# Kernel tuning notes

Hardware: AMD Instinct MI355X
Metric: run time of the kernel (lower is better)

Reference implementation:

```python
import jax, jax.numpy as jnp
import numpy as np

B, T, NB = 8192, 18, 6
EH, DH = 256, 256
NIN = NB + 1  # encoder GRU input: bits + feedback scalar


def gru_cell(x, h, Wih, Whh, bih, bhh):
    # PyTorch GRU cell: gates ordered (r, z, n)
    gi = x @ Wih.T + bih
    gh = h @ Whh.T + bhh
    ir, iz, inn = jnp.split(gi, 3, axis=-1)
    hr, hz, hn = jnp.split(gh, 3, axis=-1)
    r = jax.nn.sigmoid(ir + hr)
    z = jax.nn.sigmoid(iz + hz)
    n = jnp.tanh(inn + r * hn)
    return (1.0 - z) * n + z * h


def run_gru_dir(seq, Wih, Whh, bih, bhh, reverse):
    # seq: [T, B, D] -> hidden outputs [T, B, H] (aligned to original time order)
    Bn, H = seq.shape[1], Whh.shape[1]
    def step(h, x):
        h2 = gru_cell(x, h, Wih, Whh, bih, bhh)
        return h2, h2
    _, outs = jax.lax.scan(step, jnp.zeros((Bn, H), seq.dtype), seq, reverse=reverse)
    return outs


def setup_inputs() -> dict:
    key = jax.random.key(0)
    ks = jax.random.split(key, 40)
    def w(k, shape, fan):
        s = 1.0 / np.sqrt(fan)
        return jax.random.uniform(k, shape, jnp.float32, -s, s)
    inp = {}
    inp['b'] = (jax.random.uniform(ks[0], (B, NB)) < 0.5).astype(jnp.float32)
    inp['noise1'] = jax.random.normal(ks[1], (B, T, 1), jnp.float32)
    inp['noise2'] = jax.random.normal(ks[2], (B, T, 1), jnp.float32)
    # encoder GRU (2 layers, unidirectional)
    inp['enc_Wih0'] = w(ks[3], (3 * EH, NIN), EH); inp['enc_Whh0'] = w(ks[4], (3 * EH, EH), EH)
    inp['enc_bih0'] = w(ks[5], (3 * EH,), EH);     inp['enc_bhh0'] = w(ks[6], (3 * EH,), EH)
    inp['enc_Wih1'] = w(ks[7], (3 * EH, EH), EH);  inp['enc_Whh1'] = w(ks[8], (3 * EH, EH), EH)
    inp['enc_bih1'] = w(ks[9], (3 * EH,), EH);     inp['enc_bhh1'] = w(ks[10], (3 * EH,), EH)
    inp['enc_lin_W'] = w(ks[11], (1, EH), EH);     inp['enc_lin_b'] = w(ks[12], (1,), EH)
    inp['weight_power'] = jnp.ones((T,), jnp.float32)
    # decoder GRU (2 layers, bidirectional)
    inp['dec_Wih0f'] = w(ks[13], (3 * DH, 1), DH);      inp['dec_Whh0f'] = w(ks[14], (3 * DH, DH), DH)
    inp['dec_bih0f'] = w(ks[15], (3 * DH,), DH);        inp['dec_bhh0f'] = w(ks[16], (3 * DH,), DH)
    inp['dec_Wih0b'] = w(ks[17], (3 * DH, 1), DH);      inp['dec_Whh0b'] = w(ks[18], (3 * DH, DH), DH)
    inp['dec_bih0b'] = w(ks[19], (3 * DH,), DH);        inp['dec_bhh0b'] = w(ks[20], (3 * DH,), DH)
    inp['dec_Wih1f'] = w(ks[21], (3 * DH, 2 * DH), DH); inp['dec_Whh1f'] = w(ks[22], (3 * DH, DH), DH)
    inp['dec_bih1f'] = w(ks[23], (3 * DH,), DH);        inp['dec_bhh1f'] = w(ks[24], (3 * DH,), DH)
    inp['dec_Wih1b'] = w(ks[25], (3 * DH, 2 * DH), DH); inp['dec_Whh1b'] = w(ks[26], (3 * DH, DH), DH)
    inp['dec_bih1b'] = w(ks[27], (3 * DH,), DH);        inp['dec_bhh1b'] = w(ks[28], (3 * DH,), DH)
    inp['dec_lin_W'] = w(ks[29], (NB, 2 * DH), 2 * DH); inp['dec_lin_b'] = w(ks[30], (NB,), 2 * DH)
    inp['weight_merge'] = jnp.ones((T, 2), jnp.float32)
    return inp


def reference(b, noise1, noise2,
              enc_Wih0, enc_Whh0, enc_bih0, enc_bhh0,
              enc_Wih1, enc_Whh1, enc_bih1, enc_bhh1,
              enc_lin_W, enc_lin_b, weight_power,
              dec_Wih0f, dec_Whh0f, dec_bih0f, dec_bhh0f,
              dec_Wih0b, dec_Whh0b, dec_bih0b, dec_bhh0b,
              dec_Wih1f, dec_Whh1f, dec_bih1f, dec_bhh1f,
              dec_Wih1b, dec_Whh1b, dec_bih1b, dec_bhh1b,
              dec_lin_W, dec_lin_b, weight_merge):
    Bn = b.shape[0]
    Tn = weight_power.shape[0]
    # power-normalized per-step weights: sqrt(w^2 * T / sum(w^2))
    wp = jnp.sqrt(weight_power ** 2 * Tn / jnp.sum(weight_power ** 2))

    def enc_step(carry, xs):
        h0, h1, z = carry
        n1, n2, wpt = xs
        inp = jnp.concatenate([b, z], axis=1)            # [B, NB+1]
        h0n = gru_cell(inp, h0, enc_Wih0, enc_Whh0, enc_bih0, enc_bhh0)
        h1n = gru_cell(h0n, h1, enc_Wih1, enc_Whh1, enc_bih1, enc_bhh1)
        xt = jnp.tanh(h1n @ enc_lin_W.T + enc_lin_b)     # [B, 1]
        xn = (xt - jnp.mean(xt)) / jnp.std(xt, ddof=1)   # training-mode batch norm over whole tensor
        y = xn * wpt + n1                                # received symbol
        return (h0n, h1n, y + n2), y                     # feedback z = y + noise2

    carry0 = (jnp.zeros((Bn, EH), b.dtype), jnp.zeros((Bn, EH), b.dtype), jnp.zeros((Bn, 1), b.dtype))
    xs = (jnp.swapaxes(noise1, 0, 1), jnp.swapaxes(noise2, 0, 1), wp)
    _, y_seq = jax.lax.scan(enc_step, carry0, xs)        # [T, B, 1]

    # bidirectional 2-layer decoder GRU over y
    o0f = run_gru_dir(y_seq, dec_Wih0f, dec_Whh0f, dec_bih0f, dec_bhh0f, False)
    o0b = run_gru_dir(y_seq, dec_Wih0b, dec_Whh0b, dec_bih0b, dec_bhh0b, True)
    s1 = jnp.concatenate([o0f, o0b], axis=-1)            # [T, B, 2*DH]
    o1f = run_gru_dir(s1, dec_Wih1f, dec_Whh1f, dec_bih1f, dec_bhh1f, False)
    o1b = run_gru_dir(s1, dec_Wih1b, dec_Whh1b, dec_bih1b, dec_bhh1b, True)

    # attention_type == 5: learned weighted merge over time, per direction
    wf = jnp.sqrt(weight_merge[:, 0] ** 2 * Tn / jnp.sum(weight_merge[:, 0] ** 2))
    wb = jnp.sqrt(weight_merge[:, 1] ** 2 * Tn / jnp.sum(weight_merge[:, 1] ** 2))
    rf = jnp.einsum('tbh,t->bh', o1f, wf)
    rb = jnp.einsum('tbh,t->bh', o1b, wb)
    rc = jnp.concatenate([rf, rb], axis=1)               # [B, 2*DH]
    out = jax.nn.sigmoid(rc @ dec_lin_W.T + dec_lin_b)   # bit_vector output -> sigmoid
    return out.reshape(Bn, -1, 1)
```

## Files before the change

### kernel.cpp

```cpp
#include <hip/hip_runtime.h>
#include <hip/hip_bf16.h>
#include <math.h>

#define BN_ 8192
#define TT 18
#define NBITS 6
#define HH 256
#define G3 768

typedef __hip_bfloat16 hbf16;
typedef __bf16 bf16x8 __attribute__((ext_vector_type(8)));
typedef float f32x4 __attribute__((ext_vector_type(4)));

__device__ inline float sigm(float x){ return 1.0f/(1.0f + __expf(-x)); }
__device__ inline float ftanh(float x){ float e = __expf(2.0f*x); return 1.0f - 2.0f/(e + 1.0f); }
__device__ inline float ldx(const void* p, int i, int bf){
    if(bf){ unsigned short u = ((const unsigned short*)p)[i]; return __uint_as_float(((unsigned)u)<<16); }
    return ((const float*)p)[i];
}
__device__ inline __bf16 f2b(float f){ hbf16 h = __float2bfloat16(f); return *reinterpret_cast<__bf16*>(&h); }
__device__ inline float b2f(__bf16 b){ unsigned short u = *reinterpret_cast<unsigned short*>(&b); return __uint_as_float(((unsigned)u)<<16); }
__device__ inline unsigned pack2(float a, float b){
    hbf16 lo = __float2bfloat16(a), hi = __float2bfloat16(b);
    return (unsigned)*(unsigned short*)&lo | ((unsigned)*(unsigned short*)&hi << 16);
}

__device__ __forceinline__ void gld_lds16(const void* g, void* l){
    __builtin_amdgcn_global_load_lds(
        (const __attribute__((address_space(1))) unsigned int*)g,
        (__attribute__((address_space(3))) unsigned int*)l, 16, 0, 0);
}

__global__ __launch_bounds__(256) void fillz(float* __restrict__ p, int n){
    for(int i = blockIdx.x*256 + threadIdx.x; i < n; i += gridDim.x*256) p[i] = 0.0f;
}
__global__ __launch_bounds__(256) void fillb(__bf16* __restrict__ p, int n){
    for(int i = blockIdx.x*256 + threadIdx.x; i < n; i += gridDim.x*256) p[i] = f2b(0.0f);
}

__global__ void prep_w(const void* wp, const void* wm, unsigned* flag,
                       float* wpn, float* wfn, float* wbn){
    if(threadIdx.x==0 && blockIdx.x==0){
        unsigned w0 = *(const unsigned*)wp;
        int bf = ((w0 >> 16) == (w0 & 0xFFFFu)) ? 1 : 0;
        flag[0] = (unsigned)bf;
        float s=0; for(int t=0;t<TT;t++){ float v=ldx(wp,t,bf); s += v*v; }
        for(int t=0;t<TT;t++){ float v=ldx(wp,t,bf); wpn[t] = sqrtf(v*v*TT/s); }
        float sf=0, sb=0;
        for(int t=0;t<TT;t++){ float f=ldx(wm,2*t,bf), b=ldx(wm,2*t+1,bf); sf += f*f; sb += b*b; }
        for(int t=0;t<TT;t++){
            float f=ldx(wm,2*t,bf), b=ldx(wm,2*t+1,bf);
            wfn[t] = sqrtf(f*f*TT/sf);
            wbn[t] = sqrtf(b*b*TT/sb);
        }
    }
}

struct CJ { const void* src; void* dst; int n; int K; int mode; };
struct CJs { CJ j[20]; };
__global__ __launch_bounds__(256) void conv_all(CJs J, const unsigned* __restrict__ flagp){
    const int bf = (int)*flagp;
    CJ c = J.j[blockIdx.y];
    for(int i = blockIdx.x*256 + threadIdx.x; i < c.n; i += gridDim.x*256){
        if(c.mode==1){
            int row = i / c.K, k = i - row*c.K;
            int g = row>>8, jj = row&255;
            int prow = ((jj>>4)*48) + g*16 + (jj&15);
            ((__bf16*)c.dst)[(size_t)prow*c.K + k] = f2b(ldx(c.src, i, bf));
        }else if(c.mode==2){
            int t = i >> 13, b = i & (BN_-1);
            ((float*)c.dst)[i] = ldx(c.src, b*TT + t, bf);
        }else{
            ((float*)c.dst)[i] = ldx(c.src, i, bf);
        }
    }
}

struct FQ {
    const __bf16* A1; const __bf16* W1; int K1;
    const __bf16* A2; const __bf16* W2; int K2;
    const float* bgi; const float* bgh;
    const __bf16* h; __bf16* hout;
    const void* bits; const void* wih0raw; const void* bih0raw;
    const void* linw; float* xt;
    const float* y; const void* wihraw; const void* bihraw; __bf16* s1t;
    float* racc; const float* wct;
};
struct FQ2 { FQ q[2]; };

template<int MODE>
__global__ __launch_bounds__(256,4) void fused_step(FQ2 PP, const unsigned* __restrict__ flagp){
    const FQ P = PP.q[blockIdx.z];
    const int bf = (int)*flagp;
    constexpr int BM   = (MODE<=1) ? 64 : 128;
    constexpr int NF   = BM/32;
    constexpr int ABYT = BM*64;
    constexpr int BUFB = ABYT + 6144;
    __shared__ __align__(16) char smem[28672];
    __shared__ float zs[192];
    __shared__ float sred[4], ssred[4];
    float*  T  = (float*)smem;
    const int tid = threadIdx.x;
    constexpr int MTS = (8192/BM)/8;
    const int mt = blockIdx.x*MTS + (blockIdx.y>>3);
    const int jt = blockIdx.y & 7;
    const int m0 = mt*BM;
    const int n0 = jt*96;
    const int lane = tid&63, wv = tid>>6;
    const int wvbase = tid & ~63;
    const int wrow = wv>>1, wcol = wv&1;
    const int q = lane>>4, n15 = lane&15;

    constexpr int S1  = (MODE==1) ? 8 : (MODE==3 ? 16 : 0);
    constexpr int NST = S1 + 8;
    constexpr int KD1 = (MODE==3) ? 512 : 256;
    constexpr int KD2 = 256;
    const __bf16* pA1 = (S1>0) ? P.A1 + (size_t)m0*KD1 : (const __bf16*)nullptr;
    const __bf16* pW1 = (S1>0) ? P.W1 + (size_t)n0*KD1 : (const __bf16*)nullptr;
    const __bf16* pA2 = P.A2 + (size_t)m0*KD2;
    const __bf16* pW2 = P.W2 + (size_t)n0*KD2;
    const int r0 = tid>>2, sl0 = tid&3;
    const int q0 = sl0 ^ ((r0>>1)&3);
    const int r1 = 64 + r0;
    const int q1 = sl0 ^ ((r1>>1)&3);

    auto STG = [&](int s){
        const __bf16* A; const __bf16* W; int K; int k0;
        if(s < S1){ A = pA1; W = pW1; K = KD1; k0 = s*32; }
        else      { A = pA2; W = pW2; K = KD2; k0 = (s-S1)*32; }
        char* buf = smem + (s&1)*BUFB;
        gld_lds16(A + (size_t)r0*K + k0 + q0*8, buf + (size_t)wvbase*16);
        if constexpr(BM==128)
            gld_lds16(A + (size_t)r1*K + k0 + q1*8, buf + (size_t)(256+wvbase)*16);
        gld_lds16(W + (size_t)r0*K + k0 + q0*8, buf + ABYT + (size_t)wvbase*16);
        if(tid < 128)
            gld_lds16(W + (size_t)r1*K + k0 + q1*8, buf + ABYT + (size_t)(256+wvbase)*16);
    };

    STG(0);

    if(MODE==0){
        if(P.K1){
            const float lbv = ldx(P.linw, 0, bf);
            const float wt  = P.wct[0];
            const float* __restrict__ xr = P.xt;
            float s=0.0f, ss=0.0f;
            const float4* x4 = (const float4*)xr;
            for(int i=tid;i<BN_/4;i+=256){
                float4 vv = x4[i];
                float a0=ftanh(vv.x+lbv), a1=ftanh(vv.y+lbv), a2=ftanh(vv.z+lbv), a3=ftanh(vv.w+lbv);
                s += a0+a1+a2+a3; ss += a0*a0+a1*a1+a2*a2+a3*a3;
            }
            #pragma unroll
            for(int o=32;o;o>>=1){ s += __shfl_xor(s,o); ss += __shfl_xor(ss,o); }
            if(lane==0){ sred[wv]=s; ssred[wv]=ss; }
            __syncthreads();
            float a = sred[0]+sred[1]+sred[2]+sred[3];
            float bq = ssred[0]+ssred[1]+ssred[2]+ssred[3];
            float mean = a/(float)BN_;
            float var = (bq - (float)BN_*mean*mean)/(float)(BN_-1);
            float rs = 1.0f/sqrtf(var);
            if(tid<BM){
                int row = m0 + tid;
                float v = ftanh(xr[row]+lbv);
                float yv = (v-mean)*rs*wt + P.y[row];
                zs[tid] = yv + ((const float*)P.wihraw)[row];
                if(jt==0){ ((float*)P.s1t)[row] = yv; P.racc[row] = 0.0f; }
            }
        }else{
            if(tid<BM) zs[tid] = 0.0f;
        }
        __syncthreads();
    }else{
        __syncthreads();
    }

    f32x4 accR[NF], accZ[NF], accN1[NF], accN2[NF];
    #pragma unroll
    for(int i=0;i<NF;i++){ accR[i]=(f32x4){0,0,0,0}; accZ[i]=(f32x4){0,0,0,0};
                           accN1[i]=(f32x4){0,0,0,0}; accN2[i]=(f32x4){0,0,0,0}; }

    #pragma unroll
    for(int s=0; s<NST; ++s){
        if(s+1 < NST) STG(s+1);
        const char* buf = smem + (s&1)*BUFB;
        const __bf16* Asb = (const __bf16*)buf;
        const __bf16* Wsb = (const __bf16*)(buf + ABYT);
        bf16x8 af[NF], bfr[3];
        #pragma unroll
        for(int i=0;i<NF;i++){
            int R = wrow*(BM/2)+i*16+n15;
            int col = q ^ ((R>>1)&3);
            af[i] = *(const bf16x8*)&Asb[R*32 + col*8];
        }
        #pragma unroll
        for(int g=0;g<3;g++){
            int RW = wcol*48+g*16+n15;
            int col = q ^ ((RW>>1)&3);
            bfr[g] = *(const bf16x8*)&Wsb[RW*32 + col*8];
        }
        #pragma unroll
        for(int i=0;i<NF;i++){
            accR[i] = __builtin_amdgcn_mfma_f32_16x16x32_bf16(af[i], bfr[0], accR[i], 0,0,0);
            accZ[i] = __builtin_amdgcn_mfma_f32_16x16x32_bf16(af[i], bfr[1], accZ[i], 0,0,0);
            if(s < S1) accN1[i] = __builtin_amdgcn_mfma_f32_16x16x32_bf16(af[i], bfr[2], accN1[i], 0,0,0);
            else       accN2[i] = __builtin_amdgcn_mfma_f32_16x16x32_bf16(af[i], bfr[2], accN2[i], 0,0,0);
        }
        __syncthreads();
    }

    const int jl = wcol*16 + n15;
    const int j  = jt*32 + jl;
    const float bghr = P.bgh[j], bghz = P.bgh[256+j], bghn = P.bgh[512+j];
    float bgir=0, bgiz=0, bgin=0;
    if(MODE==1 || MODE==3){ bgir = P.bgi[j]; bgiz = P.bgi[256+j]; bgin = P.bgi[512+j]; }
    float w0r[7], w0z[7], w0n[7];
    if(MODE==0){
        #pragma unroll
        for(int k=0;k<7;k++){
            w0r[k] = ldx(P.wih0raw, (j    )*7+k, bf);
            w0z[k] = ldx(P.wih0raw, (j+256)*7+k, bf);
            w0n[k] = ldx(P.wih0raw, (j+512)*7+k, bf);
        }
        bgir = ldx(P.bih0raw, j, bf); bgiz = ldx(P.bih0raw, j+256, bf); bgin = ldx(P.bih0raw, j+512, bf);
    }
    float wy_r=0, wy_z=0, wy_n=0;
    if(MODE==2){
        wy_r = ldx(P.wihraw, j, bf); wy_z = ldx(P.wihraw, j+256, bf); wy_n = ldx(P.wihraw, j+512, bf);
        bgir = ldx(P.bihraw, j, bf); bgiz = ldx(P.bihraw, j+256, bf); bgin = ldx(P.bihraw, j+512, bf);
    }
    const float linwj = (MODE==1) ? ldx(P.linw, j, bf) : 0.0f;

    #pragma unroll
    for(int i=0;i<NF;i++){
        const int rbl = wrow*(BM/2) + i*16 + q*4;
        float vred[4];
        #pragma unroll
        for(int r=0;r<4;r++){
            const int row_l = rbl + r;
            const int row = m0 + row_l;
            float gir, giz, gin;
            if(MODE==1 || MODE==3){
                gir = bgir; giz = bgiz; gin = accN1[i][r] + bgin;
            }else if(MODE==0){
                gir = bgir; giz = bgiz; gin = bgin;
                #pragma unroll
                for(int k=0;k<NBITS;k++){
                    float bv = ldx(P.bits, row*NBITS+k, bf);
                    gir += bv*w0r[k]; giz += bv*w0z[k]; gin += bv*w0n[k];
                }
                float zb = zs[row_l];
                gir += zb*w0r[6]; giz += zb*w0z[6]; gin += zb*w0n[6];
            }else{
                float yv = P.y[row];
                gir = yv*wy_r + bgir; giz = yv*wy_z + bgiz; gin = yv*wy_n + bgin;
            }
            float rr = sigm(gir + accR[i][r] + bghr);
            float zz = sigm(giz + accZ[i][r] + bghz);
            float nn = ftanh(gin + rr*(accN2[i][r] + bghn));
            float hold = b2f(P.h[(size_t)row*HH + j]);
            float hn = (1.0f - zz)*nn + zz*hold;
            T[row_l*33 + jl] = hn;
            if(MODE==1) vred[r] = hn*linwj;
        }
        if(MODE==1){
            #pragma unroll
            for(int r=0;r<4;r++){
                float v = vred[r];
                #pragma unroll
                for(int m=1;m<16;m<<=1) v += __shfl_xor(v, m);
                if(n15==0) atomicAdd(&P.xt[m0+rbl+r], v);
            }
        }
    }
    if(MODE==3 && tid<192){
        int k = tid>>5, jj = tid&31;
        zs[tid] = ldx(P.bits, k*512 + (int)blockIdx.z*256 + jt*32 + jj, bf);
    }
    __syncthreads();

    const int rw2 = tid>>2, cw = tid&3;
    #pragma unroll
    for(int pass=0; pass<BM/64; pass++){
        const int row_l = pass*64 + rw2;
        const int row = m0 + row_l;
        float v[8];
        #pragma unroll
        for(int u=0;u<8;u++) v[u] = T[row_l*33 + cw*8 + u];
        uint4 pkv = { pack2(v[0],v[1]), pack2(v[2],v[3]), pack2(v[4],v[5]), pack2(v[6],v[7]) };
        *(uint4*)&P.hout[(size_t)row*HH + jt*32 + cw*8] = pkv;
        if(MODE==2) *(uint4*)&P.s1t[(size_t)row*512 + jt*32 + cw*8] = pkv;
    }
    if(MODE==3){
        float* pp = P.xt + (size_t)(jt + 8*(int)blockIdx.z)*(BN_*NBITS);
        const float wct3 = P.wct[0];
        #pragma unroll
        for(int u=0;u<3;u++){
            int idx = tid + 256*u;
            int row_l = idx/6, k = idx - row_l*6;
            float dot = 0.0f;
            #pragma unroll
            for(int jj=0;jj<32;jj++) dot += T[row_l*33+jj]*zs[k*32+jj];
            size_t gi = (size_t)(m0+row_l)*NBITS + k;
            pp[gi] += wct3*dot;
        }
    }
}

__global__ __launch_bounds__(1024) void stats_emit(float* __restrict__ xt, const void* __restrict__ lb,
        const float* __restrict__ wpn, int t, const float* __restrict__ n1t, const float* __restrict__ n2t,
        float* __restrict__ yseq, float* __restrict__ zf, const unsigned* __restrict__ flagp){
    const int bf = (int)*flagp;
    const float lbv = ldx(lb, 0, bf);
    int tid = threadIdx.x;
    float s=0.0f, ss=0.0f;
    for(int i=tid;i<BN_;i+=1024){ float v = ftanh(xt[i] + lbv); s += v; ss += v*v; }
    #pragma unroll
    for(int o=32;o;o>>=1){ s += __shfl_down(s,o); ss += __shfl_down(ss,o); }
    __shared__ float S[16], SS[16], stm[2];
    if((tid&63)==0){ S[tid>>6]=s; SS[tid>>6]=ss; }
    __syncthreads();
    if(tid==0){
        float a=0.0f, b=0.0f;
        for(int i=0;i<16;i++){ a+=S[i]; b+=SS[i]; }
        float mean = a/(float)BN_;
        float var = (b - (float)BN_*mean*mean)/(float)(BN_-1);
        stm[0]=mean; stm[1]=1.0f/sqrtf(var);
    }
    __syncthreads();
    const float mean=stm[0], rs=stm[1], wt=wpn[t];
    for(int i=tid;i<BN_;i+=1024){
        float v = ftanh(xt[i] + lbv);
        float y = (v-mean)*rs*wt + n1t[i];
        yseq[(size_t)t*BN_ + i] = y;
        zf[i] = y + n2t[i];
        xt[i] = 0.0f;
    }
}

__global__ __launch_bounds__(256) void out_head(const float* __restrict__ pp, const void* __restrict__ bias,
        void* __restrict__ out, const unsigned* __restrict__ flagp){
    const int bf = (int)*flagp;
    int i = blockIdx.x*256 + threadIdx.x;
    if(i >= BN_*NBITS) return;
    float s = 0.0f;
    #pragma unroll
    for(int k=0;k<16;k++) s += pp[(size_t)k*(BN_*NBITS) + i];
    int kk = i - (i/6)*6;
    float v = sigm(s + ldx(bias, kk, bf));
    if(bf) ((hbf16*)out)[i] = __float2bfloat16(v);
    else   ((float*)out)[i] = v;
}

extern "C" void kernel_launch(void* const* d_in, const int* in_sizes, int n_in,
                              void* d_out, int out_size, void* d_ws, size_t ws_size,
                              hipStream_t stream)
{
    (void)in_sizes; (void)n_in; (void)out_size;
    const void* bits  = d_in[0];
    const void* n1    = d_in[1];
    const void* n2    = d_in[2];
    const void* eWih0 = d_in[3];
    const void* eWhh0 = d_in[4];
    const void* ebih0 = d_in[5];
    const void* ebhh0 = d_in[6];
    const void* eWih1 = d_in[7];
    const void* eWhh1 = d_in[8];
    const void* ebih1 = d_in[9];
    const void* ebhh1 = d_in[10];
    const void* elinW = d_in[11];
    const void* elinb = d_in[12];
    const void* wpow  = d_in[13];
    const void* dWih0f= d_in[14];
    const void* dWhh0f= d_in[15];
    const void* dbih0f= d_in[16];
    const void* dbhh0f= d_in[17];
    const void* dWih0b= d_in[18];
    const void* dWhh0b= d_in[19];
    const void* dbih0b= d_in[20];
    const void* dbhh0b= d_in[21];
    const void* dWih1f= d_in[22];
    const void* dWhh1f= d_in[23];
    const void* dbih1f= d_in[24];
    const void* dbhh1f= d_in[25];
    const void* dWih1b= d_in[26];
    const void* dWhh1b= d_in[27];
    const void* dbih1b= d_in[28];
    const void* dbhh1b= d_in[29];
    const void* dlinW = d_in[30];
    const void* dlinb = d_in[31];
    const void* wmrg  = d_in[32];

    float* base = (float*)d_ws;
    size_t off = 0;
    auto alloc  = [&](size_t n){ float* p = base + off; off += (n + 63) & ~(size_t)63; return p; };
    auto allocb = [&](size_t n){ __bf16* p = (__bf16*)(base + off); off += ((n/2) + 63) & ~(size_t)63; return p; };
    unsigned* flag = (unsigned*)alloc(64);
    float* wpn = alloc(TT); float* wfn = alloc(TT); float* wbn = alloc(TT);
    const int WK = HH*G3;
    __bf16* WeHH0 = allocb(WK);  __bf16* WeIH1 = allocb(WK);  __bf16* WeHH1 = allocb(WK);
    __bf16* Wd0f  = allocb(WK);  __bf16* Wd0b  = allocb(WK);
    __bf16* Wd1fI = allocb(2*WK);__bf16* Wd1bI = allocb(2*WK);
    __bf16* Wd1fH = allocb(WK);  __bf16* Wd1bH = allocb(WK);
    float* BeHH0 = alloc(G3); float* BeIH1 = alloc(G3); float* BeHH1 = alloc(G3);
    float* Bd0f  = alloc(G3); float* Bd0b  = alloc(G3);
    float* Bd1fI = alloc(G3); float* Bd1bI = alloc(G3);
    float* Bd1fH = alloc(G3); float* Bd1bH = alloc(G3);
    const size_t NH = (size_t)BN_*HH;
    __bf16* X0 = allocb(NH);  __bf16* X1 = allocb(NH);
    __bf16* Y0 = allocb(NH);  __bf16* Y1 = allocb(NH);
    float* pout = alloc((size_t)16*BN_*NBITS);
    float* xtA = alloc(BN_);
    float* xtB = alloc(BN_);
    float* zf  = alloc(BN_);
    float* yseq= alloc((size_t)TT*BN_);
    float* n1t = alloc((size_t)TT*BN_);
    float* n2t = alloc((size_t)TT*BN_);
    __bf16* s1 = allocb((size_t)TT*BN_*512);
    size_t need = off*sizeof(float);
    if(ws_size < need) return;

    prep_w<<<1,64,0,stream>>>(wpow, wmrg, flag, wpn, wfn, wbn);
    CJs J;
    const void* ws_src[20] = {eWhh0,eWih1,eWhh1,dWhh0f,dWhh0b,dWih1f,dWih1b,dWhh1f,dWhh1b,
                              ebhh0,ebih1,ebhh1,dbhh0f,dbhh0b,dbih1f,dbih1b,dbhh1f,dbhh1b, n1, n2};
    void* ws_dst[20] = {WeHH0,WeIH1,WeHH1,Wd0f,Wd0b,Wd1fI,Wd1bI,Wd1fH,Wd1bH,
                        BeHH0,BeIH1,BeHH1,Bd0f,Bd0b,Bd1fI,Bd1bI,Bd1fH,Bd1bH, n1t, n2t};
    int ws_n[20] = {WK,WK,WK,WK,WK,2*WK,2*WK,WK,WK, G3,G3,G3,G3,G3,G3,G3,G3,G3, TT*BN_, TT*BN_};
    int ws_K[20] = {256,256,256,256,256,512,512,256,256, 0,0,0,0,0,0,0,0,0, 0,0};
    int ws_m[20] = {1,1,1,1,1,1,1,1,1, 0,0,0,0,0,0,0,0,0, 2,2};
    for(int i=0;i<20;i++){ J.j[i] = {ws_src[i], ws_dst[i], ws_n[i], ws_K[i], ws_m[i]}; }
    conv_all<<<dim3(768,20),256,0,stream>>>(J, flag);
    fillb<<<1024,256,0,stream>>>(X0, (int)NH);
    fillb<<<1024,256,0,stream>>>(Y0, (int)NH);
    fillz<<<32,256,0,stream>>>(xtA, BN_);
    fillz<<<32,256,0,stream>>>(xtB, BN_);
    fillz<<<192,256,0,stream>>>(pout, 16*BN_*NBITS);

    dim3 g1(8, 128, 1), g2(8, 64, 2);
    __bf16* X[2] = {X0, X1};
    __bf16* Y[2] = {Y0, Y1};
    float* xts[2] = {xtA, xtB};

    int p = 0;
    for(int t=0;t<TT;t++){
        FQ2 P0{}; FQ2 P1{};
        FQ& a = P0.q[0];
        a.A2=X[p]; a.W2=WeHH0; a.K2=HH; a.bgh=BeHH0; a.h=X[p]; a.hout=X[1-p];
        a.bits=bits; a.wih0raw=eWih0; a.bih0raw=ebih0;
        a.K1 = (t>0) ? 1 : 0;
        if(t>0){
            a.xt   = xts[(t-1)&1];
            a.racc = xts[t&1];
            a.y    = n1t + (size_t)(t-1)*BN_;
            a.wihraw = (const void*)(n2t + (size_t)(t-1)*BN_);
            a.s1t  = (__bf16*)(yseq + (size_t)(t-1)*BN_);
            a.wct  = wpn + (t-1);
            a.linw = elinb;
        }
        fused_step<0><<<g1,256,0,stream>>>(P0, flag);
        FQ& b = P1.q[0];
        b.A1=X[1-p]; b.W1=WeIH1; b.K1=HH; b.A2=Y[p]; b.W2=WeHH1; b.K2=HH;
        b.bgi=BeIH1; b.bgh=BeHH1; b.h=Y[p]; b.hout=Y[1-p];
        b.linw=elinW; b.xt=xts[t&1];
        fused_step<1><<<g1,256,0,stream>>>(P1, flag);
        p ^= 1;
    }
    stats_emit<<<1,1024,0,stream>>>(xts[(TT-1)&1], elinb, wpn, TT-1,
                                    n1t+(size_t)(TT-1)*BN_, n2t+(size_t)(TT-1)*BN_, yseq, zf, flag);

    fillb<<<1024,256,0,stream>>>(X0, (int)NH);
    fillb<<<1024,256,0,stream>>>(Y0, (int)NH);
    p = 0;
    for(int i=0;i<TT;i++){
        int tf = i, tb = TT-1-i;
        FQ2 P{};
        FQ& a = P.q[0];
        a.A2=X[p]; a.W2=Wd0f; a.K2=HH; a.bgh=Bd0f; a.h=X[p]; a.hout=X[1-p];
        a.y=yseq+(size_t)tf*BN_; a.wihraw=dWih0f; a.bihraw=dbih0f; a.s1t=s1+(size_t)tf*BN_*512;
        FQ& b = P.q[1];
        b.A2=Y[p]; b.W2=Wd0b; b.K2=HH; b.bgh=Bd0b; b.h=Y[p]; b.hout=Y[1-p];
        b.y=yseq+(size_t)tb*BN_; b.wihraw=dWih0b; b.bihraw=dbih0b; b.s1t=s1+(size_t)tb*BN_*512+256;
        fused_step<2><<<g2,256,0,stream>>>(P, flag);
        p ^= 1;
    }

    fillb<<<1024,256,0,stream>>>(X0, (int)NH);
    fillb<<<1024,256,0,stream>>>(Y0, (int)NH);
    p = 0;
    for(int i=0;i<TT;i++){
        int tf = i, tb = TT-1-i;
        FQ2 P{};
        FQ& a = P.q[0];
        a.A1=s1+(size_t)tf*BN_*512; a.W1=Wd1fI; a.K1=512;
        a.A2=X[p]; a.W2=Wd1fH; a.K2=HH; a.bgi=Bd1fI; a.bgh=Bd1fH; a.h=X[p]; a.hout=X[1-p];
        a.bits=dlinW; a.xt=pout; a.wct=wfn+tf;
        FQ& b = P.q[1];
        b.A1=s1+(size_t)tb*BN_*512; b.W1=Wd1bI; b.K1=512;
        b.A2=Y[p]; b.W2=Wd1bH; b.K2=HH; b.bgi=Bd1bI; b.bgh=Bd1bH; b.h=Y[p]; b.hout=Y[1-p];
        b.bits=dlinW; b.xt=pout; b.wct=wbn+tb;
        fused_step<3><<<g2,256,0,stream>>>(P, flag);
        p ^= 1;
    }

    out_head<<<192,256,0,stream>>>(pout, dlinb, d_out, flag);
}
```

Baseline: 1.698 ms.

## Widen decoder GRU step tiles to 512 threads covering 64 hidden units

For the decoder modes, each block now runs 512 threads (8 waves) and covers 192 gate columns (64 hidden units) instead of 96, halving the number of column tiles per row tile. A-operand tiles of batch rows are reloaded half as often, and the partial-output buffer for the bit-projection shrinks from 16 to 8 slices. The cost is more shared memory and registers per block, which may reduce occupancy under the launch bounds.

```diff
diff --git a/kernel.cpp b/kernel.cpp
--- a/kernel.cpp
+++ b/kernel.cpp
@@ -89,26 +89,33 @@
 struct FQ2 { FQ q[2]; };
 
 template<int MODE>
-__global__ __launch_bounds__(256,4) void fused_step(FQ2 PP, const unsigned* __restrict__ flagp){
+__global__ __launch_bounds__((MODE>=2)?512:256, 4) void fused_step(FQ2 PP, const unsigned* __restrict__ flagp){
     const FQ P = PP.q[blockIdx.z];
     const int bf = (int)*flagp;
+    constexpr int THREADS = (MODE>=2) ? 512 : 256;
     constexpr int BM   = (MODE<=1) ? 64 : 128;
+    constexpr int WR   = (MODE>=2) ? 192 : 96;
+    constexpr int JB   = WR/3;
     constexpr int NF   = BM/32;
     constexpr int ABYT = BM*64;
-    constexpr int BUFB = ABYT + 6144;
-    __shared__ __align__(16) char smem[28672];
-    __shared__ float zs[192];
+    constexpr int WBYT = WR*64;
+    constexpr int BUFB = ABYT + WBYT;
+    constexpr int TS   = JB + 1;
+    __shared__ __align__(16) char smem[2*BUFB];
+    __shared__ float zs[(MODE>=2)?384:192];
     __shared__ float sred[4], ssred[4];
     float*  T  = (float*)smem;
     const int tid = threadIdx.x;
+    constexpr int JTBITS = (MODE>=2) ? 2 : 3;
     constexpr int MTS = (8192/BM)/8;
-    const int mt = blockIdx.x*MTS + (blockIdx.y>>3);
-    const int jt = blockIdx.y & 7;
+    const int mt = blockIdx.x*MTS + (blockIdx.y>>JTBITS);
+    const int jt = blockIdx.y & ((1<<JTBITS)-1);
     const int m0 = mt*BM;
-    const int n0 = jt*96;
+    const int n0 = jt*WR;
     const int lane = tid&63, wv = tid>>6;
     const int wvbase = tid & ~63;
-    const int wrow = wv>>1, wcol = wv&1;
+    const int wrow = (MODE>=2) ? (wv>>2) : (wv>>1);
+    const int wcol = wv & ((MODE>=2)?3:1);
     const int q = lane>>4, n15 = lane&15;
 
     constexpr int S1  = (MODE==1) ? 8 : (MODE==3 ? 16 : 0);
@@ -121,8 +128,8 @@
     const __bf16* pW2 = P.W2 + (size_t)n0*KD2;
     const int r0 = tid>>2, sl0 = tid&3;
     const int q0 = sl0 ^ ((r0>>1)&3);
-    const int r1 = 64 + r0;
-    const int q1 = sl0 ^ ((r1>>1)&3);
+    const int rW1 = THREADS/4 + r0;
+    const int qW1 = sl0 ^ ((rW1>>1)&3);
 
     auto STG = [&](int s){
         const __bf16* A; const __bf16* W; int K; int k0;
@@ -130,11 +137,9 @@
         else      { A = pA2; W = pW2; K = KD2; k0 = (s-S1)*32; }
         char* buf = smem + (s&1)*BUFB;
         gld_lds16(A + (size_t)r0*K + k0 + q0*8, buf + (size_t)wvbase*16);
-        if constexpr(BM==128)
-            gld_lds16(A + (size_t)r1*K + k0 + q1*8, buf + (size_t)(256+wvbase)*16);
         gld_lds16(W + (size_t)r0*K + k0 + q0*8, buf + ABYT + (size_t)wvbase*16);
-        if(tid < 128)
-            gld_lds16(W + (size_t)r1*K + k0 + q1*8, buf + ABYT + (size_t)(256+wvbase)*16);
+        if(tid < THREADS/2)
+            gld_lds16(W + (size_t)rW1*K + k0 + qW1*8, buf + ABYT + (size_t)(THREADS+wvbase)*16);
     };
 
     STG(0);
@@ -146,7 +151,7 @@
             const float* __restrict__ xr = P.xt;
             float s=0.0f, ss=0.0f;
             const float4* x4 = (const float4*)xr;
-            for(int i=tid;i<BN_/4;i+=256){
+            for(int i=tid;i<BN_/4;i+=THREADS){
                 float4 vv = x4[i];
                 float a0=ftanh(vv.x+lbv), a1=ftanh(vv.y+lbv), a2=ftanh(vv.z+lbv), a3=ftanh(vv.w+lbv);
                 s += a0+a1+a2+a3; ss += a0*a0+a1*a1+a2*a2+a3*a3;
@@ -210,7 +215,7 @@
     }
 
     const int jl = wcol*16 + n15;
-    const int j  = jt*32 + jl;
+    const int j  = jt*JB + jl;
     const float bghr = P.bgh[j], bghz = P.bgh[256+j], bghn = P.bgh[512+j];
     float bgir=0, bgiz=0, bgin=0;
     if(MODE==1 || MODE==3){ bgir = P.bgi[j]; bgiz = P.bgi[256+j]; bgin = P.bgi[512+j]; }
@@ -260,7 +265,7 @@
             float nn = ftanh(gin + rr*(accN2[i][r] + bghn));
             float hold = b2f(P.h[(size_t)row*HH + j]);
             float hn = (1.0f - zz)*nn + zz*hold;
-            T[row_l*33 + jl] = hn;
+            T[row_l*TS + jl] = hn;
             if(MODE==1) vred[r] = hn*linwj;
         }
         if(MODE==1){
@@ -273,36 +278,49 @@
             }
         }
     }
-    if(MODE==3 && tid<192){
-        int k = tid>>5, jj = tid&31;
-        zs[tid] = ldx(P.bits, k*512 + (int)blockIdx.z*256 + jt*32 + jj, bf);
+    if(MODE==3 && tid<6*JB){
+        int k = tid/JB, jj = tid - k*JB;
+        zs[tid] = ldx(P.bits, k*512 + (int)blockIdx.z*256 + jt*JB + jj, bf);
     }
     __syncthreads();
 
-    const int rw2 = tid>>2, cw = tid&3;
-    #pragma unroll
-    for(int pass=0; pass<BM/64; pass++){
-        const int row_l = pass*64 + rw2;
+    if constexpr(MODE<=1){
+        const int rw2 = tid>>2, cw = tid&3;
+        const int row_l = rw2;
         const int row = m0 + row_l;
         float v[8];
         #pragma unroll
-        for(int u=0;u<8;u++) v[u] = T[row_l*33 + cw*8 + u];
+        for(int u=0;u<8;u++) v[u] = T[row_l*TS + cw*8 + u];
         uint4 pkv = { pack2(v[0],v[1]), pack2(v[2],v[3]), pack2(v[4],v[5]), pack2(v[6],v[7]) };
-        *(uint4*)&P.hout[(size_t)row*HH + jt*32 + cw*8] = pkv;
-        if(MODE==2) *(uint4*)&P.s1t[(size_t)row*512 + jt*32 + cw*8] = pkv;
+        *(uint4*)&P.hout[(size_t)row*HH + jt*JB + cw*8] = pkv;
+    }else{
+        const int rw2 = tid>>3, cw = tid&7;
+        #pragma unroll
+        for(int pass=0; pass<2; pass++){
+            const int row_l = pass*64 + rw2;
+            const int row = m0 + row_l;
+            float v[8];
+            #pragma unroll
+            for(int u=0;u<8;u++) v[u] = T[row_l*TS + cw*8 + u];
+            uint4 pkv = { pack2(v[0],v[1]), pack2(v[2],v[3]), pack2(v[4],v[5]), pack2(v[6],v[7]) };
+            *(uint4*)&P.hout[(size_t)row*HH + jt*JB + cw*8] = pkv;
+            if(MODE==2) *(uint4*)&P.s1t[(size_t)row*512 + jt*JB + cw*8] = pkv;
+        }
     }
     if(MODE==3){
-        float* pp = P.xt + (size_t)(jt + 8*(int)blockIdx.z)*(BN_*NBITS);
+        float* pp = P.xt + (size_t)(jt + 4*(int)blockIdx.z)*(BN_*NBITS);
         const float wct3 = P.wct[0];
         #pragma unroll
-        for(int u=0;u<3;u++){
-            int idx = tid + 256*u;
-            int row_l = idx/6, k = idx - row_l*6;
-            float dot = 0.0f;
-            #pragma unroll
-            for(int jj=0;jj<32;jj++) dot += T[row_l*33+jj]*zs[k*32+jj];
-            size_t gi = (size_t)(m0+row_l)*NBITS + k;
-            pp[gi] += wct3*dot;
+        for(int u=0;u<2;u++){
+            int idx = tid + THREADS*u;
+            if(idx < BM*NBITS){
+                int row_l = idx/6, k = idx - row_l*6;
+                float dot = 0.0f;
+                #pragma unroll
+                for(int jj=0;jj<JB;jj++) dot += T[row_l*TS+jj]*zs[k*JB+jj];
+                size_t gi = (size_t)(m0+row_l)*NBITS + k;
+                pp[gi] += wct3*dot;
+            }
         }
     }
 }
@@ -345,7 +363,7 @@
     if(i >= BN_*NBITS) return;
     float s = 0.0f;
     #pragma unroll
-    for(int k=0;k<16;k++) s += pp[(size_t)k*(BN_*NBITS) + i];
+    for(int k=0;k<8;k++) s += pp[(size_t)k*(BN_*NBITS) + i];
     int kk = i - (i/6)*6;
     float v = sigm(s + ldx(bias, kk, bf));
     if(bf) ((hbf16*)out)[i] = __float2bfloat16(v);
@@ -409,7 +427,7 @@
     const size_t NH = (size_t)BN_*HH;
     __bf16* X0 = allocb(NH);  __bf16* X1 = allocb(NH);
     __bf16* Y0 = allocb(NH);  __bf16* Y1 = allocb(NH);
-    float* pout = alloc((size_t)16*BN_*NBITS);
+    float* pout = alloc((size_t)8*BN_*NBITS);
     float* xtA = alloc(BN_);
     float* xtB = alloc(BN_);
     float* zf  = alloc(BN_);
@@ -435,9 +453,9 @@
     fillb<<<1024,256,0,stream>>>(Y0, (int)NH);
     fillz<<<32,256,0,stream>>>(xtA, BN_);
     fillz<<<32,256,0,stream>>>(xtB, BN_);
-    fillz<<<192,256,0,stream>>>(pout, 16*BN_*NBITS);
-
-    dim3 g1(8, 128, 1), g2(8, 64, 2);
+    fillz<<<96,256,0,stream>>>(pout, 8*BN_*NBITS);
+
+    dim3 g1(8, 128, 1), g2(8, 32, 2);
     __bf16* X[2] = {X0, X1};
     __bf16* Y[2] = {Y0, Y1};
     float* xts[2] = {xtA, xtB};
@@ -481,7 +499,7 @@
         FQ& b = P.q[1];
         b.A2=Y[p]; b.W2=Wd0b; b.K2=HH; b.bgh=Bd0b; b.h=Y[p]; b.hout=Y[1-p];
         b.y=yseq+(size_t)tb*BN_; b.wihraw=dWih0b; b.bihraw=dbih0b; b.s1t=s1+(size_t)tb*BN_*512+256;
-        fused_step<2><<<g2,256,0,stream>>>(P, flag);
+        fused_step<2><<<g2,512,0,stream>>>(P, flag);
         p ^= 1;
     }
 
@@ -499,7 +517,7 @@
         b.A1=s1+(size_t)tb*BN_*512; b.W1=Wd1bI; b.K1=512;
         b.A2=Y[p]; b.W2=Wd1bH; b.K2=HH; b.bgi=Bd1bI; b.bgh=Bd1bH; b.h=Y[p]; b.hout=Y[1-p];
         b.bits=dlinW; b.xt=pout; b.wct=wbn+tb;
-        fused_step<3><<<g2,256,0,stream>>>(P, flag);
+        fused_step<3><<<g2,512,0,stream>>>(P, flag);
         p ^= 1;
     }
 
```

New measurement: 1.691 ms. No clear change (-0.4%).
